# Kernel optimization log

Measured on AMD Instinct MI355X. Metric: run time of the kernel, lower is better.

Reference implementation:

```python
import jax, jax.numpy as jnp
import numpy as np
from jax import lax

B, C, H, W = 4, 64, 128, 128
G, K, CO = 8, 3, 64
KK = K * K
MC = G * KK  # mask channels = 72


def _conv3x3(x, w, b):
    # standard 3x3 conv, stride 1, padding 1, NCHW
    y = lax.conv_general_dilated(x, w, (1, 1), ((1, 1), (1, 1)),
                                 dimension_numbers=('NCHW', 'OIHW', 'NCHW'))
    return y + b[None, :, None, None]


def _deform_conv2d(x, offset, mask, w, b):
    """Modulated deformable conv (DCNv2), stride=1, padding=1, dilation=1.
    offset: [B, 2*G*KK, H, W] interpreted as [B, G, KK, 2(dy,dx), H, W] (torchvision layout).
    mask:   [B, G*KK, H, W].
    w: [Co, C/G, K, K], b: [Co].
    """
    Bn, Cn, Hn, Wn = x.shape
    Co, Cg, Kh, Kw = w.shape
    Gn = Cn // Cg
    KKn = Kh * Kw
    Ho, Wo = Hn, Wn  # stride 1, pad 1, k 3

    off = offset.reshape(Bn, Gn, KKn, 2, Ho, Wo)
    dy, dx = off[:, :, :, 0], off[:, :, :, 1]
    m = mask.reshape(Bn, Gn, 1, KKn, Ho, Wo)

    kh = (jnp.arange(KKn) // Kw).astype(x.dtype)  # kernel row index
    kw = (jnp.arange(KKn) % Kw).astype(x.dtype)
    hh = jnp.arange(Ho, dtype=x.dtype)
    ww = jnp.arange(Wo, dtype=x.dtype)
    # sampling positions: h - pad + kh*dil + dy  -> [B,G,KK,Ho,Wo]
    py = hh[None, None, None, :, None] - 1.0 + kh[None, None, :, None, None] + dy
    px = ww[None, None, None, None, :] - 1.0 + kw[None, None, :, None, None] + dx

    y0 = jnp.floor(py); x0 = jnp.floor(px)
    ly = py - y0; lx = px - x0
    y0i = y0.astype(jnp.int32); x0i = x0.astype(jnp.int32)
    y1i = y0i + 1; x1i = x0i + 1

    xg = x.reshape(Bn, Gn, Cg, Hn * Wn)

    def corner(yi, xi, wgt):
        valid = ((yi >= 0) & (yi < Hn) & (xi >= 0) & (xi < Wn)).astype(x.dtype)
        idx = (jnp.clip(yi, 0, Hn - 1) * Wn + jnp.clip(xi, 0, Wn - 1))
        idx = idx.reshape(Bn, Gn, 1, KKn * Ho * Wo)
        v = jnp.take_along_axis(xg, idx, axis=3).reshape(Bn, Gn, Cg, KKn, Ho, Wo)
        return v * (wgt * valid)[:, :, None]

    val = (corner(y0i, x0i, (1.0 - ly) * (1.0 - lx))
           + corner(y0i, x1i, (1.0 - ly) * lx)
           + corner(y1i, x0i, ly * (1.0 - lx))
           + corner(y1i, x1i, ly * lx))
    val = val * m  # modulation

    wr = w.reshape(Gn, Co // Gn, Cg, KKn)
    out = jnp.einsum('bgckhw,gock->bgohw', val, wr).reshape(Bn, Co, Ho, Wo)
    return out + b[None, :, None, None]


def setup_inputs() -> dict:
    key = jax.random.key(0)
    ks = jax.random.split(key, 8)
    f = lambda k, s, sc=1.0: jax.random.normal(k, s, dtype=jnp.float32) * sc
    return {
        'x': f(ks[0], (B, C, H, W)),
        'share_with_feat': f(ks[1], (B, C, H, W)),
        'offset_feat': f(ks[2], (B, C, H, W)),
        # conv_offset_mask: C -> 3*G*KK (zero-init in original; small random here)
        'w_om': f(ks[3], (3 * MC, C, 3, 3), 0.02),
        'b_om': jnp.zeros((3 * MC,), jnp.float32),
        'w_em1': f(ks[4], (C, 2 * C, 3, 3), 0.05),
        'b_em1': jnp.zeros((C,), jnp.float32),
        'w_em2': f(ks[5], (MC, C, 3, 3), 0.05),
        'b_em2': jnp.zeros((MC,), jnp.float32),
        # deform conv weight: [Co, C/G, 3, 3]
        'w_dc': f(ks[6], (CO, C // G, 3, 3), 0.05),
        'b_dc': f(ks[7], (CO,), 0.05),
    }


def reference(x, share_with_feat, offset_feat, w_om, b_om, w_em1, b_em1,
              w_em2, b_em2, w_dc, b_dc):
    om = _conv3x3(offset_feat, w_om, b_om)
    o1, o2, mask_x = jnp.split(om, 3, axis=1)
    offset = jnp.concatenate([o1, o2], axis=1)
    mask_x = jax.nn.sigmoid(mask_x)
    x_deform = _deform_conv2d(x, offset, mask_x, w_dc, b_dc)
    # extra_mask=True branch
    em = _conv3x3(jnp.concatenate([share_with_feat, offset_feat], axis=1), w_em1, b_em1)
    em = jnp.where(em >= 0, em, 0.1 * em)  # LeakyReLU(0.1)
    em = jax.nn.sigmoid(_conv3x3(em, w_em2, b_em2))
    share_deform = _deform_conv2d(share_with_feat, offset, em, w_dc, b_dc)
    return (x_deform, share_deform)
```

## Files before the change

kernel.cpp:

```cpp
#include <hip/hip_runtime.h>
#include <math.h>

#define BB 4
#define CC 64
#define HH 128
#define WW 128
#define GG 8
#define COO 64
#define HWC (HH*WW)

#define DPAD 12
#define DROW 26

typedef float f32x4 __attribute__((ext_vector_type(4)));
typedef __bf16 bf16x8 __attribute__((ext_vector_type(8)));

__device__ __forceinline__ unsigned short bf16_rn(float f) {
    unsigned int u = __float_as_uint(f);
    unsigned int r = (u + 0x7fffu + ((u >> 16) & 1u)) >> 16;
    return (unsigned short)r;
}
__device__ __forceinline__ float b2f(unsigned short u) {
    return __uint_as_float(((unsigned int)u) << 16);
}

__global__ __launch_bounds__(256) void pack_inputs_kernel(
    const float* __restrict__ x, const float* __restrict__ share,
    const float* __restrict__ offf,
    unsigned int* __restrict__ xs, unsigned short* __restrict__ sc16,
    unsigned short* __restrict__ oc16)
{
    __shared__ unsigned short lds[64][66];
    const int b = blockIdx.y;
    const int pix0 = blockIdx.x * 64;
    const int t = threadIdx.x;
    const int p = t & 63, q = t >> 6;
    const int pl = t & 63, cg = t >> 6;

#pragma unroll
    for (int i = 0; i < 16; i++) {
        int c = i * 4 + q;
        size_t idx = ((size_t)b * 64 + c) * HWC + pix0 + p;
        unsigned short sb = bf16_rn(share[idx]);
        lds[c][p] = sb;
        xs[idx] = (unsigned int)bf16_rn(x[idx]) | ((unsigned int)sb << 16);
    }
    __syncthreads();
    {
        unsigned int u[8];
#pragma unroll
        for (int j = 0; j < 8; j++) {
            unsigned int lo = lds[cg * 16 + 2 * j][pl];
            unsigned int hi = lds[cg * 16 + 2 * j + 1][pl];
            u[j] = lo | (hi << 16);
        }
        unsigned int* dst = (unsigned int*)(sc16 + ((size_t)(b * 4 + cg) * HWC + pix0 + pl) * 16);
        *(uint4*)dst = make_uint4(u[0], u[1], u[2], u[3]);
        *(uint4*)(dst + 4) = make_uint4(u[4], u[5], u[6], u[7]);
    }
    __syncthreads();

#pragma unroll
    for (int i = 0; i < 16; i++) {
        int c = i * 4 + q;
        lds[c][p] = bf16_rn(offf[((size_t)b * 64 + c) * HWC + pix0 + p]);
    }
    __syncthreads();
    {
        unsigned int u[8];
#pragma unroll
        for (int j = 0; j < 8; j++) {
            unsigned int lo = lds[cg * 16 + 2 * j][pl];
            unsigned int hi = lds[cg * 16 + 2 * j + 1][pl];
            u[j] = lo | (hi << 16);
        }
        unsigned int* dst = (unsigned int*)(oc16 + ((size_t)(b * 4 + cg) * HWC + pix0 + pl) * 16);
        *(uint4*)dst = make_uint4(u[0], u[1], u[2], u[3]);
        *(uint4*)(dst + 4) = make_uint4(u[4], u[5], u[6], u[7]);
    }
}

__device__ __forceinline__ void pack_w_one(const float* __restrict__ w,
                                           unsigned short* __restrict__ wp,
                                           int Cout, int COP, int CinTot, int idx) {
    int j    = idx & 7;
    int lane = (idx >> 3) & 63;
    int rem  = idx >> 9;
    int ncob = COP >> 4;
    int cob  = rem % ncob;
    int t    = rem / ncob;
    int seg  = t / 18;
    int tt   = t % 18;
    int kk   = tt >> 1;
    int ks   = tt & 1;
    int co   = cob * 16 + (lane & 15);
    int kl   = ((lane >> 4) << 3) + j;
    int cg   = ks * 2 + (kl >> 4);
    int ci   = kl & 15;
    int cin  = seg * 64 + cg * 16 + ci;
    float v = (co < Cout) ? w[((size_t)co * CinTot + cin) * 9 + kk] : 0.f;
    wp[idx] = bf16_rn(v);
}

__global__ void pack_w_all_kernel(const float* __restrict__ w_om, unsigned short* __restrict__ wp_om,
                                  const float* __restrict__ w_em1, unsigned short* __restrict__ wp_em1,
                                  const float* __restrict__ w_em2, unsigned short* __restrict__ wp_em2) {
    int i = blockIdx.x * 256 + threadIdx.x;
    if (i < 147456) {
        pack_w_one(w_om, wp_om, 216, 256, 64, i);
    } else if (i < 147456 + 73728) {
        pack_w_one(w_em1, wp_em1, 64, 64, 128, i - 147456);
    } else if (i < 147456 + 73728 + 73728) {
        pack_w_one(w_em2, wp_em2, 72, 128, 64, i - 147456 - 73728);
    }
}

template<int NSEG, int COP, int XS>
__global__ __launch_bounds__(256) void conv_mfma_kernel(
    const unsigned short* __restrict__ in0,
    const unsigned short* __restrict__ in1,
    const unsigned short* __restrict__ wp,
    const float* __restrict__ bias,
    void* __restrict__ out,
    int Cout, int out_mode, int act)
{
    constexpr int PXT = 128 / XS;
    constexpr int NT  = PXT / 16;
    constexpr int PXW = PXT + 2;
    constexpr int NE  = 4 * 6 * PXW;
    constexpr int NCB = COP >> 4;
    __shared__ __align__(16) unsigned short slds[NE * 16];
    __shared__ __align__(16) unsigned short wlds[18 * 1024];

    const int tix  = threadIdx.x;
    const int lane = tix & 63;
    const int wid  = tix >> 6;
    int tmp = blockIdx.x;
    const int xsp = tmp % XS; tmp /= XS;
    const int rb  = tmp & 31;
    const int b   = tmp >> 5;
    const int r0  = rb * 4;
    const int r   = r0 + wid;
    const int px0 = xsp * PXT;
    const int cb0 = blockIdx.y * 2;
    const int co0 = blockIdx.y * 32;

    f32x4 acc[2][NT];
#pragma unroll
    for (int cob = 0; cob < 2; cob++)
#pragma unroll
        for (int nt = 0; nt < NT; nt++)
#pragma unroll
            for (int rg = 0; rg < 4; rg++) acc[cob][nt][rg] = 0.f;

    const int pxl  = lane & 15;
    const int kgrp = lane >> 4;
    const int cglh = lane >> 5;
    const int cil0 = (kgrp & 1) * 8;
    const unsigned short* lp = slds +
        ((size_t)(cglh * 6 + wid) * PXW + 1 + pxl) * 16 + cil0;
    const unsigned short* ap = wlds + lane * 8;

#pragma unroll
    for (int seg = 0; seg < NSEG; seg++) {
        const unsigned short* inb = (seg ? in1 : in0) + (size_t)b * 4 * HWC * 16;
        if (seg) __syncthreads();

#pragma unroll
        for (int i = 0; i < 9; i++) {
            const int idx = tix + i * 256;
            const int tl  = idx >> 7;
            const int c   = idx & 127;
            const uint4 v = *(const uint4*)(wp +
                ((size_t)((seg * 18 + tl) * NCB + cb0) * 512) + c * 8);
            *(uint4*)(wlds + (size_t)tl * 1024 + c * 8) = v;
        }

#pragma unroll
        for (int i = 0; i < (NE + 255) / 256; i++) {
            const int e = tix + i * 256;
            if (i < NE / 256 || e < NE) {
                const int cg  = e / (6 * PXW);
                const int rem = e - cg * (6 * PXW);
                const int row = rem / PXW;
                const int px  = rem - row * PXW;
                const int iy = r0 - 1 + row;
                const int ix = px0 - 1 + px;
                const bool valid = ((unsigned)iy < (unsigned)HH) && ((unsigned)ix < (unsigned)WW);
                const int iyc = min(max(iy, 0), HH - 1);
                const int ixc = min(max(ix, 0), WW - 1);
                const uint4* src = (const uint4*)(inb + ((size_t)cg * HWC + (size_t)iyc * WW + ixc) * 16);
                uint4 v0, v1;
                if (valid) { v0 = src[0]; v1 = src[1]; }
                else       { v0 = make_uint4(0u, 0u, 0u, 0u); v1 = v0; }
                uint4* dst = (uint4*)(slds + (size_t)e * 16);
                dst[0] = v0; dst[1] = v1;
            }
        }
        __syncthreads();

#pragma unroll
        for (int t = 0; t < 18; t++) {
            const int kk = t >> 1, ks = t & 1;
            const int kh = kk / 3, kw = kk % 3;
            bf16x8 af[2];
#pragma unroll
            for (int cob = 0; cob < 2; cob++)
                af[cob] = *(const bf16x8*)(ap + t * 1024 + cob * 512);
            bf16x8 bf[NT];
#pragma unroll
            for (int nt = 0; nt < NT; nt++)
                bf[nt] = *(const bf16x8*)(lp +
                    ((ks * 12 + kh) * PXW + nt * 16 + kw - 1) * 16);
#pragma unroll
            for (int cob = 0; cob < 2; cob++)
#pragma unroll
                for (int nt = 0; nt < NT; nt++)
                    acc[cob][nt] = __builtin_amdgcn_mfma_f32_16x16x32_bf16(
                        af[cob], bf[nt], acc[cob][nt], 0, 0, 0);
        }
    }

#pragma unroll
    for (int cob = 0; cob < 2; cob++) {
#pragma unroll
        for (int nt = 0; nt < NT; nt++) {
#pragma unroll
            for (int rg = 0; rg < 4; rg++) {
                const int co = co0 + cob * 16 + kgrp * 4 + rg;
                if (co < Cout) {
                    float v = acc[cob][nt][rg] + bias[co];
                    if (act == 1)      v = (v >= 0.f) ? v : 0.1f * v;
                    else if (act == 2) v = 1.f / (1.f + __expf(-v));
                    else if (act == 3 && co >= 144) v = 1.f / (1.f + __expf(-v));
                    const int pix = r * WW + px0 + nt * 16 + pxl;
                    if (out_mode == 2)
                        ((unsigned short*)out)[((size_t)b * Cout + co) * HWC + pix] = bf16_rn(v);
                    else
                        ((unsigned short*)out)[((size_t)(b * 4 + (co >> 4)) * HWC + pix) * 16 + (co & 15)] = bf16_rn(v);
                }
            }
        }
    }
}

__global__ __launch_bounds__(256) void deform_fused_kernel(
    const unsigned int* __restrict__ xs,
    const unsigned short* __restrict__ om, const unsigned short* __restrict__ em,
    const float* __restrict__ wdc, const float* __restrict__ bdc,
    float* __restrict__ outx, float* __restrict__ outs)
{
    __shared__ __align__(16) unsigned int lds[24 * DROW * DPAD];

    const int bg = blockIdx.x >> 6;
    const int b = bg >> 3, g = bg & 7;
    const int tile = blockIdx.x & 63;
    const int r0 = (tile >> 3) << 4;
    const int c0 = (tile & 7) << 4;
    const int tx = threadIdx.x & 15, ty = threadIdx.x >> 4;
    const int h = r0 + ty, w = c0 + tx;
    const int wr0 = r0 - 4, wc0 = c0 - 4;

    const unsigned int* xsb = xs + ((size_t)b * 64 + g * 8) * HWC;

#pragma unroll
    for (int i = 0; i < 18; i++) {
        unsigned int slot = (unsigned int)threadIdx.x + i * 256u;
        unsigned int sx = slot % 24u;
        unsigned int t2 = slot / 24u;
        unsigned int sy = t2 % 24u;
        unsigned int c  = t2 / 24u;
        int iy = min(max(wr0 + (int)sy, 0), HH - 1);
        int ix = min(max(wc0 + (int)sx, 0), WW - 1);
        lds[(sy * DROW + sx) * DPAD + c] = xsb[(size_t)c * HWC + iy * WW + ix];
    }

    __syncthreads();

    const int pix = h * WW + w;
    const unsigned short* omb = om + (size_t)b * 216 * HWC + pix + (size_t)g * 18 * HWC;
    const unsigned short* mmb = om + (size_t)b * 216 * HWC + pix + (size_t)(144 + g * 9) * HWC;
    const unsigned short* emb = em + (size_t)b * 72 * HWC + pix + (size_t)g * 9 * HWC;

    float accx[8], accs[8];
#pragma unroll
    for (int o = 0; o < 8; o++) { accx[o] = 0.f; accs[o] = 0.f; }

#pragma unroll
    for (int kk = 0; kk < 9; kk++) {
        const float dy = b2f(omb[(size_t)(kk * 2) * HWC]);
        const float dx = b2f(omb[(size_t)(kk * 2 + 1) * HWC]);
        const float m1 = b2f(mmb[(size_t)kk * HWC]);
        const float m2 = b2f(emb[(size_t)kk * HWC]);

        const float py = (float)(h - 1 + kk / 3) + dy;
        const float px = (float)(w - 1 + kk % 3) + dx;
        const float y0f = floorf(py), x0f = floorf(px);
        const float ly = py - y0f, lx = px - x0f;
        const int y0 = (int)y0f, x0 = (int)x0f;
        const int y1 = y0 + 1, x1 = x0 + 1;
        const bool vy0 = (y0 >= 0) && (y0 < HH), vy1 = (y1 >= 0) && (y1 < HH);
        const bool vx0 = (x0 >= 0) && (x0 < WW), vx1 = (x1 >= 0) && (x1 < WW);
        float w00 = (1.f - ly) * (1.f - lx); if (!(vy0 && vx0)) w00 = 0.f;
        float w01 = (1.f - ly) * lx;         if (!(vy0 && vx1)) w01 = 0.f;
        float w10 = ly * (1.f - lx);         if (!(vy1 && vx0)) w10 = 0.f;
        float w11 = ly * lx;                 if (!(vy1 && vx1)) w11 = 0.f;
        const int cy0 = min(max(y0, 0), HH - 1), cy1 = min(max(y1, 0), HH - 1);
        const int cx0 = min(max(x0, 0), WW - 1), cx1 = min(max(x1, 0), WW - 1);

        const int sy0 = cy0 - wr0, sy1 = cy1 - wr0;
        const int sx0 = cx0 - wc0, sx1 = cx1 - wc0;
        const bool inw = (sy0 >= 0) && (sy1 < 24) && (sx0 >= 0) && (sx1 < 24);

        const float* wk = wdc + (size_t)g * 8 * 8 * 9 + kk;

        if (__builtin_expect(inw, 1)) {
            const int p00 = (sy0 * DROW + sx0) * DPAD, p01 = (sy0 * DROW + sx1) * DPAD;
            const int p10 = (sy1 * DROW + sx0) * DPAD, p11 = (sy1 * DROW + sx1) * DPAD;
#pragma unroll
            for (int ch = 0; ch < 2; ch++) {
                uint4 qa = *(const uint4*)(lds + p00 + ch * 4);
                uint4 qb = *(const uint4*)(lds + p01 + ch * 4);
                uint4 qc = *(const uint4*)(lds + p10 + ch * 4);
                uint4 qd = *(const uint4*)(lds + p11 + ch * 4);
                const unsigned int ua[4] = {qa.x, qa.y, qa.z, qa.w};
                const unsigned int ub[4] = {qb.x, qb.y, qb.z, qb.w};
                const unsigned int uc[4] = {qc.x, qc.y, qc.z, qc.w};
                const unsigned int ud[4] = {qd.x, qd.y, qd.z, qd.w};
#pragma unroll
                for (int j = 0; j < 4; j++) {
                    const int c = ch * 4 + j;
                    float x00 = __uint_as_float(ua[j] << 16), s00 = __uint_as_float(ua[j] & 0xffff0000u);
                    float x01 = __uint_as_float(ub[j] << 16), s01 = __uint_as_float(ub[j] & 0xffff0000u);
                    float x10 = __uint_as_float(uc[j] << 16), s10 = __uint_as_float(uc[j] & 0xffff0000u);
                    float x11 = __uint_as_float(ud[j] << 16), s11 = __uint_as_float(ud[j] & 0xffff0000u);
                    float vx = w00 * x00; vx = fmaf(w01, x01, vx); vx = fmaf(w10, x10, vx); vx = fmaf(w11, x11, vx);
                    float vs = w00 * s00; vs = fmaf(w01, s01, vs); vs = fmaf(w10, s10, vs); vs = fmaf(w11, s11, vs);
                    vx *= m1;
                    vs *= m2;
#pragma unroll
                    for (int o = 0; o < 8; o++) {
                        const float wv = wk[(size_t)(o * 8 + c) * 9];
                        accx[o] = fmaf(vx, wv, accx[o]);
                        accs[o] = fmaf(vs, wv, accs[o]);
                    }
                }
            }
        } else {
            const int i00 = cy0 * WW + cx0, i01 = cy0 * WW + cx1;
            const int i10 = cy1 * WW + cx0, i11 = cy1 * WW + cx1;
#pragma unroll
            for (int c = 0; c < 8; c++) {
                const unsigned int* xc = xsb + (size_t)c * HWC;
                unsigned int a = xc[i00], bq = xc[i01], cq = xc[i10], dq = xc[i11];
                float x00 = __uint_as_float(a << 16),  s00 = __uint_as_float(a & 0xffff0000u);
                float x01 = __uint_as_float(bq << 16), s01 = __uint_as_float(bq & 0xffff0000u);
                float x10 = __uint_as_float(cq << 16), s10 = __uint_as_float(cq & 0xffff0000u);
                float x11 = __uint_as_float(dq << 16), s11 = __uint_as_float(dq & 0xffff0000u);
                float vx = w00 * x00; vx = fmaf(w01, x01, vx); vx = fmaf(w10, x10, vx); vx = fmaf(w11, x11, vx);
                float vs = w00 * s00; vs = fmaf(w01, s01, vs); vs = fmaf(w10, s10, vs); vs = fmaf(w11, s11, vs);
                vx *= m1;
                vs *= m2;
#pragma unroll
                for (int o = 0; o < 8; o++) {
                    const float wv = wk[(size_t)(o * 8 + c) * 9];
                    accx[o] = fmaf(vx, wv, accx[o]);
                    accs[o] = fmaf(vs, wv, accs[o]);
                }
            }
        }
    }

#pragma unroll
    for (int o = 0; o < 8; o++) {
        const float bv = bdc[g * 8 + o];
        outx[((size_t)(b * COO + g * 8 + o)) * HWC + pix] = accx[o] + bv;
        outs[((size_t)(b * COO + g * 8 + o)) * HWC + pix] = accs[o] + bv;
    }
}

extern "C" void kernel_launch(void* const* d_in, const int* in_sizes, int n_in,
                              void* d_out, int out_size, void* d_ws, size_t ws_size,
                              hipStream_t stream) {
    const float* x      = (const float*)d_in[0];
    const float* share  = (const float*)d_in[1];
    const float* offf   = (const float*)d_in[2];
    const float* w_om   = (const float*)d_in[3];
    const float* b_om   = (const float*)d_in[4];
    const float* w_em1  = (const float*)d_in[5];
    const float* b_em1  = (const float*)d_in[6];
    const float* w_em2  = (const float*)d_in[7];
    const float* b_em2  = (const float*)d_in[8];
    const float* w_dc   = (const float*)d_in[9];
    const float* b_dc   = (const float*)d_in[10];

    unsigned int* xs = (unsigned int*)d_ws;
    unsigned short* us = (unsigned short*)(xs + 4194304);
    unsigned short* sc16   = us;
    unsigned short* oc16   = sc16 + 4194304;
    unsigned short* emm    = oc16 + 4194304;
    unsigned short* om_b   = emm + 4194304;
    unsigned short* em_b   = om_b + 14155776;
    unsigned short* wp_om  = em_b + 4718592;
    unsigned short* wp_em1 = wp_om + 147456;
    unsigned short* wp_em2 = wp_em1 + 73728;

    float* outx = (float*)d_out;
    float* outs = outx + 4194304;

    dim3 blk(256);

    pack_inputs_kernel<<<dim3(HWC / 64, BB), blk, 0, stream>>>(x, share, offf, xs, sc16, oc16);
    pack_w_all_kernel<<<(147456 + 73728 + 73728) / 256, blk, 0, stream>>>(
        w_om, wp_om, w_em1, wp_em1, w_em2, wp_em2);

    conv_mfma_kernel<1, 256, 4><<<dim3(BB * 32 * 4, 7), blk, 0, stream>>>(
        oc16, nullptr, wp_om, b_om, om_b, 216, 2, 3);
    conv_mfma_kernel<2, 64, 4><<<dim3(BB * 32 * 4, 2), blk, 0, stream>>>(
        sc16, oc16, wp_em1, b_em1, emm, 64, 3, 1);
    conv_mfma_kernel<1, 128, 4><<<dim3(BB * 32 * 4, 3), blk, 0, stream>>>(
        emm, nullptr, wp_em2, b_em2, em_b, 72, 2, 2);

    deform_fused_kernel<<<dim3(BB * GG * 64), blk, 0, stream>>>(
        xs, om_b, em_b, w_dc, b_dc, outx, outs);
}
```

Baseline: 291.2 us.

## Interleave offset and mask channels per group for vectorized deform loads

The offset/mask conv and the extra-mask conv now write their bf16 outputs into a per-(batch, group) pixel-interleaved buffer of 36 slots, split into four 8-wide planes plus one 4-wide plane. The deform kernel then fetches all offsets and both masks for a pixel with five vector loads issued before the LDS fill, replacing 36 strided scalar loads. This is meant to cut memory transactions and latency in the deform kernel. In exchange, the conv epilogues do scattered 2-byte stores with extra index math, and the em1 conv out_mode is renumbered from 3 to 0.

After: 299.7 us. 1.03x slower.

```diff
diff --git a/kernel.cpp b/kernel.cpp
--- a/kernel.cpp
+++ b/kernel.cpp
@@ -12,6 +12,8 @@
 #define DPAD 12
 #define DROW 26
 
+#define PS8 4194304
+
 typedef float f32x4 __attribute__((ext_vector_type(4)));
 typedef __bf16 bf16x8 __attribute__((ext_vector_type(8)));
 
@@ -22,6 +24,9 @@
 }
 __device__ __forceinline__ float b2f(unsigned short u) {
     return __uint_as_float(((unsigned int)u) << 16);
+}
+__device__ __forceinline__ float ddx(unsigned int wrd, int half) {
+    return half ? __uint_as_float(wrd & 0xffff0000u) : __uint_as_float(wrd << 16);
 }
 
 __global__ __launch_bounds__(256) void pack_inputs_kernel(
@@ -234,10 +239,23 @@
                     else if (act == 2) v = 1.f / (1.f + __expf(-v));
                     else if (act == 3 && co >= 144) v = 1.f / (1.f + __expf(-v));
                     const int pix = r * WW + px0 + nt * 16 + pxl;
-                    if (out_mode == 2)
-                        ((unsigned short*)out)[((size_t)b * Cout + co) * HWC + pix] = bf16_rn(v);
-                    else
+                    if (out_mode == 0) {
                         ((unsigned short*)out)[((size_t)(b * 4 + (co >> 4)) * HWC + pix) * 16 + (co & 15)] = bf16_rn(v);
+                    } else {
+                        int gg, slot;
+                        if (out_mode == 3) {
+                            if (co < 144) { gg = co / 18; slot = co - gg * 18; }
+                            else { int cm = co - 144; gg = cm / 9; slot = 18 + cm - gg * 9; }
+                        } else {
+                            gg = co / 9; slot = 27 + co - gg * 9;
+                        }
+                        unsigned short* ddp = (unsigned short*)out;
+                        const size_t base = (size_t)((b << 3) + gg) * HWC + pix;
+                        if (slot < 32)
+                            ddp[(size_t)(slot >> 3) * PS8 + base * 8 + (slot & 7)] = bf16_rn(v);
+                        else
+                            ddp[4 * (size_t)PS8 + base * 4 + (slot - 32)] = bf16_rn(v);
+                    }
                 }
             }
         }
@@ -246,7 +264,7 @@
 
 __global__ __launch_bounds__(256) void deform_fused_kernel(
     const unsigned int* __restrict__ xs,
-    const unsigned short* __restrict__ om, const unsigned short* __restrict__ em,
+    const unsigned short* __restrict__ dd,
     const float* __restrict__ wdc, const float* __restrict__ bdc,
     float* __restrict__ outx, float* __restrict__ outs)
 {
@@ -260,8 +278,17 @@
     const int tx = threadIdx.x & 15, ty = threadIdx.x >> 4;
     const int h = r0 + ty, w = c0 + tx;
     const int wr0 = r0 - 4, wc0 = c0 - 4;
+    const int pix = h * WW + w;
 
     const unsigned int* xsb = xs + ((size_t)b * 64 + g * 8) * HWC;
+
+    const unsigned short* db = dd + ((size_t)bg * HWC + pix) * 8;
+    uint4 q[4];
+    q[0] = *(const uint4*)(db);
+    q[1] = *(const uint4*)(db + PS8);
+    q[2] = *(const uint4*)(db + 2 * (size_t)PS8);
+    q[3] = *(const uint4*)(db + 3 * (size_t)PS8);
+    const uint2 q4 = *(const uint2*)(dd + 4 * (size_t)PS8 + ((size_t)bg * HWC + pix) * 4);
 
 #pragma unroll
     for (int i = 0; i < 18; i++) {
@@ -277,21 +304,19 @@
 
     __syncthreads();
 
-    const int pix = h * WW + w;
-    const unsigned short* omb = om + (size_t)b * 216 * HWC + pix + (size_t)g * 18 * HWC;
-    const unsigned short* mmb = om + (size_t)b * 216 * HWC + pix + (size_t)(144 + g * 9) * HWC;
-    const unsigned short* emb = em + (size_t)b * 72 * HWC + pix + (size_t)g * 9 * HWC;
-
     float accx[8], accs[8];
 #pragma unroll
     for (int o = 0; o < 8; o++) { accx[o] = 0.f; accs[o] = 0.f; }
 
 #pragma unroll
     for (int kk = 0; kk < 9; kk++) {
-        const float dy = b2f(omb[(size_t)(kk * 2) * HWC]);
-        const float dx = b2f(omb[(size_t)(kk * 2 + 1) * HWC]);
-        const float m1 = b2f(mmb[(size_t)kk * HWC]);
-        const float m2 = b2f(emb[(size_t)kk * HWC]);
+        const int s_dy = 2 * kk, s_dx = 2 * kk + 1, s_m1 = 18 + kk, s_m2 = 27 + kk;
+        const float dy = ddx(((const unsigned int*)&q[s_dy >> 3])[(s_dy & 7) >> 1], s_dy & 1);
+        const float dx = ddx(((const unsigned int*)&q[s_dx >> 3])[(s_dx & 7) >> 1], s_dx & 1);
+        const float m1 = ddx(((const unsigned int*)&q[s_m1 >> 3])[(s_m1 & 7) >> 1], s_m1 & 1);
+        float m2;
+        if (s_m2 < 32) m2 = ddx(((const unsigned int*)&q[s_m2 >> 3])[(s_m2 & 7) >> 1], s_m2 & 1);
+        else           m2 = ddx(((s_m2 - 32) >> 1) ? q4.y : q4.x, s_m2 & 1);
 
         const float py = (float)(h - 1 + kk / 3) + dy;
         const float px = (float)(w - 1 + kk % 3) + dx;
@@ -399,9 +424,8 @@
     unsigned short* sc16   = us;
     unsigned short* oc16   = sc16 + 4194304;
     unsigned short* emm    = oc16 + 4194304;
-    unsigned short* om_b   = emm + 4194304;
-    unsigned short* em_b   = om_b + 14155776;
-    unsigned short* wp_om  = em_b + 4718592;
+    unsigned short* dd     = emm + 4194304;
+    unsigned short* wp_om  = dd + 18874368;
     unsigned short* wp_em1 = wp_om + 147456;
     unsigned short* wp_em2 = wp_em1 + 73728;
 
@@ -415,12 +439,12 @@
         w_om, wp_om, w_em1, wp_em1, w_em2, wp_em2);
 
     conv_mfma_kernel<1, 256, 4><<<dim3(BB * 32 * 4, 7), blk, 0, stream>>>(
-        oc16, nullptr, wp_om, b_om, om_b, 216, 2, 3);
+        oc16, nullptr, wp_om, b_om, dd, 216, 3, 3);
     conv_mfma_kernel<2, 64, 4><<<dim3(BB * 32 * 4, 2), blk, 0, stream>>>(
-        sc16, oc16, wp_em1, b_em1, emm, 64, 3, 1);
+        sc16, oc16, wp_em1, b_em1, emm, 64, 0, 1);
     conv_mfma_kernel<1, 128, 4><<<dim3(BB * 32 * 4, 3), blk, 0, stream>>>(
-        emm, nullptr, wp_em2, b_em2, em_b, 72, 2, 2);
+        emm, nullptr, wp_em2, b_em2, dd, 72, 4, 2);
 
     deform_fused_kernel<<<dim3(BB * GG * 64), blk, 0, stream>>>(
-        xs, om_b, em_b, w_dc, b_dc, outx, outs);
-}
+        xs, dd, w_dc, b_dc, outx, outs);
+}
```
